# Kernel tuning notes

Hardware: AMD Instinct MI355X
Metric: run time of the kernel (lower is better)

Reference implementation:

```python
import jax, jax.numpy as jnp
import numpy as np

ATOM_DIMS = [119, 4, 12, 12, 10, 6, 6, 2, 2]
OFFSETS = jnp.asarray(np.concatenate([[0], np.cumsum(ATOM_DIMS)[:-1]]), dtype=jnp.int64)
TOTAL_ROWS = int(np.sum(ATOM_DIMS))  # 173
EPS = 1e-5
PROCESSING_STEPS = 4


def setup_inputs() -> dict:
    key = jax.random.key(0)
    ks = jax.random.split(key, 20)
    N, E, G, H, ENC = 262144, 524288, 8192, 256, 128
    x = jax.random.randint(ks[0], (N, 9), 0, 2)
    edge_index = jax.random.randint(ks[1], (2, E), 0, N)
    batch = jnp.sort(jax.random.randint(ks[2], (N,), 0, G))
    s = 0.05
    inp = {
        'x': x, 'edge_index': edge_index, 'batch': batch, 'n_graphs': G,
        'atom_emb': jax.random.normal(ks[3], (TOTAL_ROWS, H)) * s,
        'W1': jax.random.normal(ks[4], (H, H)) * s, 'b1': jnp.zeros((H,)),
        'W2': jax.random.normal(ks[5], (H, H)) * s, 'b2': jnp.zeros((H,)),
        'W3': jax.random.normal(ks[6], (H, H)) * s, 'b3': jnp.zeros((H,)),
        'gamma': jnp.ones((H,)), 'beta': jnp.zeros((H,)),
        'Wi': jax.random.normal(ks[7], (4 * H, 2 * H)) * s,
        'Wh': jax.random.normal(ks[8], (4 * H, H)) * s,
        'bi': jnp.zeros((4 * H,)), 'bh': jnp.zeros((4 * H,)),
        'lin1_W': jax.random.normal(ks[9], (ENC, 2 * H)) * s, 'lin1_b': jnp.zeros((ENC,)),
        'lin2_W': jax.random.normal(ks[10], (1, ENC)) * s, 'lin2_b': jnp.zeros((1,)),
    }
    return inp


def _gcn_conv(h, W, b, src, tgt, dinv, n_nodes):
    # GCNConv: linear, then D^-1/2 (A+I) D^-1/2 aggregation, then bias
    hw = h @ W.T
    norm = dinv[src] * dinv[tgt]                      # [E]
    agg = jax.ops.segment_sum(hw[src] * norm[:, None], tgt, num_segments=n_nodes)
    agg = agg + hw * (dinv * dinv)[:, None]           # self-loop term
    return agg + b


def _batchnorm(h, gamma, beta):
    mu = jnp.mean(h, axis=0)
    var = jnp.mean((h - mu) ** 2, axis=0)
    return (h - mu) * jax.lax.rsqrt(var + EPS) * gamma + beta


def _set2set(h, batch, n_graphs, Wi, Wh, bi, bh):
    G, H = n_graphs, h.shape[1]
    q_star = jnp.zeros((G, 2 * H), dtype=h.dtype)
    hs = jnp.zeros((G, H), dtype=h.dtype)
    cs = jnp.zeros((G, H), dtype=h.dtype)
    for _ in range(PROCESSING_STEPS):
        gates = q_star @ Wi.T + hs @ Wh.T + bi + bh   # [G, 4H], torch gate order i,f,g,o
        i, f, g, o = jnp.split(gates, 4, axis=1)
        cs = jax.nn.sigmoid(f) * cs + jax.nn.sigmoid(i) * jnp.tanh(g)
        hs = jax.nn.sigmoid(o) * jnp.tanh(cs)
        q = hs                                        # [G, H]
        e = jnp.sum(h * q[batch], axis=1)             # [N]
        m = jax.ops.segment_max(e, batch, num_segments=G)
        ee = jnp.exp(e - m[batch])
        z = jax.ops.segment_sum(ee, batch, num_segments=G)
        a = ee / z[batch]                             # scatter-softmax
        r = jax.ops.segment_sum(a[:, None] * h, batch, num_segments=G)
        q_star = jnp.concatenate([q, r], axis=1)
    return q_star


def reference(x, edge_index, batch, n_graphs, atom_emb, W1, b1, W2, b2, W3, b3,
              gamma, beta, Wi, Wh, bi, bh, lin1_W, lin1_b, lin2_W, lin2_b):
    N = x.shape[0]
    src, tgt = edge_index[0], edge_index[1]
    # AtomEncoder: sum of per-column embeddings via one offset-gather
    embed = jnp.sum(atom_emb[x + OFFSETS[None, :]], axis=1)     # [N, H]
    # gcn_norm degrees (with self loops)
    deg = jax.ops.segment_sum(jnp.ones_like(tgt, dtype=embed.dtype), tgt, num_segments=N) + 1.0
    dinv = jax.lax.rsqrt(deg)
    out = jax.nn.relu(_gcn_conv(embed, W1, b1, src, tgt, dinv, N))
    out = _batchnorm(out, gamma, beta)
    out = jax.nn.relu(_gcn_conv(out, W2, b2, src, tgt, dinv, N))
    out = _batchnorm(out, gamma, beta)
    out = _gcn_conv(out, W3, b3, src, tgt, dinv, N)
    out = _set2set(out, batch, n_graphs, Wi, Wh, bi, bh)        # [G, 2H]
    out = out @ lin1_W.T + lin1_b
    out = out @ lin2_W.T + lin2_b
    return jax.nn.sigmoid(out)
```

## Files before the change

### kernel.cpp

```cpp
#include <hip/hip_runtime.h>
#include <hip/hip_bf16.h>
#include <math.h>

using u16 = unsigned short;
typedef __attribute__((ext_vector_type(8))) short short8;
typedef __attribute__((ext_vector_type(8))) _Float16 half8;
typedef __attribute__((ext_vector_type(4))) float f32x4;
typedef __attribute__((ext_vector_type(4))) u16 u16x4;

__device__ __constant__ int c_OFF[9] = {0, 119, 123, 135, 147, 157, 163, 169, 171};

__device__ __forceinline__ float h2f(u16 u) {
    _Float16 h;
    __builtin_memcpy(&h, &u, 2);
    return (float)h;
}
__device__ __forceinline__ u16 f2h(float f) {
    _Float16 h = (_Float16)f;
    u16 u;
    __builtin_memcpy(&u, &h, 2);
    return u;
}
__device__ __forceinline__ float sigf(float x) { return 1.f / (1.f + expf(-x)); }

__global__ void k_diagf(float* out, int G, float val) {
    int i = blockIdx.x * 256 + threadIdx.x;
    if (i < G) out[i] = val;
}

__global__ void k_zero_f32(float* p, int n) {
    int i = blockIdx.x * 256 + threadIdx.x;
    if (i < n) p[i] = 0.f;
}
__global__ void k_zero_u16(u16* p, int n) {
    int i = blockIdx.x * 256 + threadIdx.x;
    if (i < n) p[i] = 0;
}
__global__ void k_zero_int(int* p, int n) {
    int i = blockIdx.x * 256 + threadIdx.x;
    if (i < n) p[i] = 0;
}

__global__ void k_cvtW(const float* __restrict__ src, u16* __restrict__ dst, int n) {
    int i = blockIdx.x * 256 + threadIdx.x;
    if (i < n) dst[i] = f2h(src[i]);
}

__global__ __launch_bounds__(256) void k_embed(const int* __restrict__ x,
                                               const float* __restrict__ emb,
                                               u16* __restrict__ out, int N) {
    __shared__ int rows[72];
    int nb = blockIdx.x * 8;
    int tid = threadIdx.x;
    if (tid < 72) rows[tid] = x[(size_t)nb * 9 + tid] + c_OFF[tid % 9];
    __syncthreads();
    int ln = tid >> 5;
    int c8 = (tid & 31) * 8;
    float s0 = 0.f, s1 = 0.f, s2 = 0.f, s3 = 0.f, s4 = 0.f, s5 = 0.f, s6 = 0.f, s7 = 0.f;
#pragma unroll
    for (int c = 0; c < 9; ++c) {
        int r = rows[ln * 9 + c];
        f32x4 a = *(const f32x4*)&emb[r * 256 + c8];
        f32x4 b = *(const f32x4*)&emb[r * 256 + c8 + 4];
        s0 += a[0]; s1 += a[1]; s2 += a[2]; s3 += a[3];
        s4 += b[0]; s5 += b[1]; s6 += b[2]; s7 += b[3];
    }
    short8 o;
    o[0] = (short)f2h(s0); o[1] = (short)f2h(s1); o[2] = (short)f2h(s2); o[3] = (short)f2h(s3);
    o[4] = (short)f2h(s4); o[5] = (short)f2h(s5); o[6] = (short)f2h(s6); o[7] = (short)f2h(s7);
    *(short8*)&out[(size_t)(nb + ln) * 256 + c8] = o;
}

__global__ void k_gstart(const int* __restrict__ batch, int* __restrict__ gstart, int N, int G) {
    int i = blockIdx.x * 256 + threadIdx.x;
    if (i >= N) return;
    int b = batch[i];
    if (i == 0) {
        for (int g = 0; g <= b; ++g) gstart[g] = 0;
    } else {
        int p = batch[i - 1];
        for (int g = p + 1; g <= b; ++g) gstart[g] = i;
    }
    if (i == N - 1) {
        for (int g = b + 1; g <= G; ++g) gstart[g] = N;
    }
}

__global__ void k_count(const int* __restrict__ tgt, int* rp, int E) {
    int e = blockIdx.x * 256 + threadIdx.x;
    if (e < E) atomicAdd(&rp[tgt[e]], 1);
}

__global__ void k_dinv(const int* __restrict__ cnt, float* __restrict__ dinv, int N) {
    int i = blockIdx.x * 256 + threadIdx.x;
    if (i < N) dinv[i] = rsqrtf((float)cnt[i] + 1.f);
}

__global__ void k_scan1(int* __restrict__ rp, int* __restrict__ bsum, int N) {
    int t = threadIdx.x;
    int base = blockIdx.x * 1024 + t * 4;
    int v0 = 0, v1 = 0, v2 = 0, v3 = 0;
    if (base + 3 < N) {
        v0 = rp[base]; v1 = rp[base + 1]; v2 = rp[base + 2]; v3 = rp[base + 3];
    } else {
        if (base < N) v0 = rp[base];
        if (base + 1 < N) v1 = rp[base + 1];
        if (base + 2 < N) v2 = rp[base + 2];
    }
    int s = v0 + v1 + v2 + v3;
    int lane = t & 63, w = t >> 6;
    int x = s;
    for (int o = 1; o < 64; o <<= 1) {
        int y = __shfl_up(x, o, 64);
        if (lane >= o) x += y;
    }
    __shared__ int wsum[4];
    if (lane == 63) wsum[w] = x;
    __syncthreads();
    int woff = 0;
    for (int i = 0; i < w; ++i) woff += wsum[i];
    int excl = woff + x - s;
    if (base < N) rp[base] = excl;
    if (base + 1 < N) rp[base + 1] = excl + v0;
    if (base + 2 < N) rp[base + 2] = excl + v0 + v1;
    if (base + 3 < N) rp[base + 3] = excl + v0 + v1 + v2;
    if (t == 255) bsum[blockIdx.x] = wsum[0] + wsum[1] + wsum[2] + wsum[3];
}

__global__ void k_scan2(int* bsum, int nb) {
    int t = threadIdx.x;
    int s = (t < nb) ? bsum[t] : 0;
    int lane = t & 63, w = t >> 6;
    int x = s;
    for (int o = 1; o < 64; o <<= 1) {
        int y = __shfl_up(x, o, 64);
        if (lane >= o) x += y;
    }
    __shared__ int wsum[4];
    if (lane == 63) wsum[w] = x;
    __syncthreads();
    int woff = 0;
    for (int i = 0; i < w; ++i) woff += wsum[i];
    if (t < nb) bsum[t] = woff + x - s;
}

__global__ void k_scan3(int* __restrict__ rp, const int* __restrict__ bsum, int N) {
    int i = blockIdx.x * 256 + threadIdx.x;
    if (i < N) rp[i] += bsum[i >> 10];
}

__global__ void k_fill(const int* __restrict__ src, const int* __restrict__ tgt,
                       int* __restrict__ rp, const float* __restrict__ dinv,
                       int2* __restrict__ est, int E) {
    int e = blockIdx.x * 256 + threadIdx.x;
    if (e < E) {
        int t = tgt[e];
        int s = src[e];
        int p = atomicAdd(&rp[t], 1);
        est[p] = make_int2(s, __float_as_int(dinv[s] * dinv[t]));
    }
}

__global__ __launch_bounds__(256, 3) void k_gemm(const u16* __restrict__ p0, int rs0,
                                                 const u16* __restrict__ p1, int rs1,
                                                 const u16* __restrict__ W,
                                                 const float* __restrict__ cvec,
                                                 u16* __restrict__ out, int N) {
    __shared__ u16 As[64][260];
    __shared__ u16 Ws[256][36];
    int r0 = blockIdx.x * 64;
    int tid = threadIdx.x, lane = tid & 63, w = tid >> 6;
#pragma unroll
    for (int i = 0; i < 8; ++i) {
        int chunk = i * 256 + tid;
        int r = chunk >> 5, c8 = chunk & 31;
        const u16* sp = (c8 < 16) ? &p0[(size_t)(r0 + r) * rs0 + c8 * 8]
                                  : &p1[(size_t)(r0 + r) * rs1 + (c8 - 16) * 8];
        *(short8*)&As[r][c8 * 8] = *(const short8*)sp;
    }
    f32x4 acc[16];
#pragma unroll
    for (int o = 0; o < 16; ++o) acc[o] = f32x4{0.f, 0.f, 0.f, 0.f};
    for (int k0 = 0; k0 < 256; k0 += 32) {
        __syncthreads();
#pragma unroll
        for (int i = 0; i < 4; ++i) {
            int chunk = i * 256 + tid;
            int r = chunk >> 2, c8 = chunk & 3;
            *(short8*)&Ws[r][c8 * 8] = *(const short8*)&W[(size_t)r * 256 + k0 + c8 * 8];
        }
        __syncthreads();
        half8 af = *(const half8*)&As[w * 16 + (lane & 15)][k0 + (lane >> 4) * 8];
#pragma unroll
        for (int o = 0; o < 16; ++o) {
            half8 wf = *(const half8*)&Ws[o * 16 + (lane & 15)][(lane >> 4) * 8];
            acc[o] = __builtin_amdgcn_mfma_f32_16x16x32_f16(af, wf, acc[o], 0, 0, 0);
        }
    }
    __syncthreads();
#pragma unroll
    for (int o = 0; o < 16; ++o) {
        int col = o * 16 + (lane & 15);
        float cv = cvec ? cvec[col] : 0.f;
#pragma unroll
        for (int r = 0; r < 4; ++r) {
            int row = w * 16 + (lane >> 4) * 4 + r;
            As[row][col] = f2h(acc[o][r] + cv);
        }
    }
    __syncthreads();
#pragma unroll
    for (int i = 0; i < 8; ++i) {
        int chunk = i * 256 + tid;
        int r = chunk >> 5, c8 = chunk & 31;
        *(short8*)&out[(size_t)(r0 + r) * 256 + c8 * 8] = *(const short8*)&As[r][c8 * 8];
    }
}

template <bool RS>
__global__ __launch_bounds__(256) void k_aggh(const u16* __restrict__ src, int srs,
                                              u16* __restrict__ dst, int drs,
                                              const int* __restrict__ rp,
                                              const int2* __restrict__ est,
                                              const float* __restrict__ dinv,
                                              const float* __restrict__ biasH,
                                              float* __restrict__ statS,
                                              float* __restrict__ statQ, int N) {
    int l = threadIdx.x & 15;
    int sub = blockIdx.x * 16 + (threadIdx.x >> 4);
    int nsub = gridDim.x * 16;
    float bv[8];
#pragma unroll
    for (int k = 0; k < 8; ++k) bv[k] = biasH[l * 8 + k];
    float ss[8] = {}, qq[8] = {};
    for (int n = sub; n < N; n += nsub) {
        int start = n ? rp[n - 1] : 0;
        int end = rp[n];
        float dn = dinv[n];
        short8 hv = *(const short8*)&src[(size_t)n * srs + l * 8];
        float a[8];
#pragma unroll
        for (int k = 0; k < 8; ++k) a[k] = h2f((u16)hv[k]) * dn * dn + bv[k];
        int j = start;
        for (; j + 1 < end; j += 2) {
            int2 e0 = est[j], e1 = est[j + 1];
            float n0 = __int_as_float(e0.y), n1 = __int_as_float(e1.y);
            short8 v0 = *(const short8*)&src[(size_t)e0.x * srs + l * 8];
            short8 v1 = *(const short8*)&src[(size_t)e1.x * srs + l * 8];
#pragma unroll
            for (int k = 0; k < 8; ++k) a[k] += h2f((u16)v0[k]) * n0 + h2f((u16)v1[k]) * n1;
        }
        if (j < end) {
            int2 e0 = est[j];
            float n0 = __int_as_float(e0.y);
            short8 v0 = *(const short8*)&src[(size_t)e0.x * srs + l * 8];
#pragma unroll
            for (int k = 0; k < 8; ++k) a[k] += h2f((u16)v0[k]) * n0;
        }
        short8 o;
#pragma unroll
        for (int k = 0; k < 8; ++k) {
            if (RS) {
                a[k] = fmaxf(a[k], 0.f);
                ss[k] += a[k];
                qq[k] += a[k] * a[k];
            }
            o[k] = (short)f2h(a[k]);
        }
        *(short8*)&dst[(size_t)n * drs + l * 8] = o;
    }
    if (RS) {
        __shared__ float sh[256];
        int t = threadIdx.x;
        sh[t] = 0.f;
        __syncthreads();
#pragma unroll
        for (int k = 0; k < 8; ++k) {
            atomicAdd(&sh[l * 8 + k], ss[k]);
            atomicAdd(&sh[128 + l * 8 + k], qq[k]);
        }
        __syncthreads();
        if (t < 128)
            atomicAdd(&statS[t], sh[t]);
        else
            atomicAdd(&statQ[t - 128], sh[t]);
    }
}

__global__ void k_copyh(const u16* __restrict__ src, u16* __restrict__ dst, int N) {
    int i = blockIdx.x * 256 + threadIdx.x;
    if (i >= N * 16) return;
    int n = i >> 4, c8 = (i & 15) * 8;
    *(short8*)&dst[(size_t)n * 128 + c8] = *(const short8*)&src[(size_t)n * 256 + c8];
}

__global__ void k_bnparam(const float* __restrict__ stats, const float* __restrict__ gamma,
                          const float* __restrict__ beta, float* __restrict__ st, int N) {
    int d = threadIdx.x;
    float inv = 1.f / (float)N;
    float mu = stats[d] * inv;
    float var = fmaxf(stats[256 + d] * inv - mu * mu, 0.f);
    float sc = gamma[d] * rsqrtf(var + 1e-5f);
    st[d] = sc;
    st[256 + d] = beta[d] - mu * sc;
}

__global__ void k_fold(const float* __restrict__ W, const float* __restrict__ st,
                       u16* __restrict__ Wp, float* __restrict__ cvec) {
    __shared__ float red[256];
    int o = blockIdx.x, k = threadIdx.x;
    float w = W[o * 256 + k];
    Wp[o * 256 + k] = f2h(w * st[k]);
    red[k] = w * st[256 + k];
    __syncthreads();
    for (int s = 128; s > 0; s >>= 1) {
        if (k < s) red[k] += red[k + s];
        __syncthreads();
    }
    if (k == 0) cvec[o] = red[0];
}

__global__ __launch_bounds__(256, 2) void k_gemmf(const u16* __restrict__ A,
                                                  const u16* __restrict__ W,
                                                  const float* __restrict__ cvec,
                                                  u16* __restrict__ C, int M, int K, int O) {
    const int PAD = 8;
    __shared__ u16 As[128][64 + PAD];
    __shared__ u16 Ws[128][64 + PAD];
    int tM = blockIdx.x, tO = blockIdx.y;
    int tid = threadIdx.x;
    int lane = tid & 63, wid = tid >> 6;
    int wM = wid & 1, wO = wid >> 1;
    f32x4 acc[4][4] = {};
    size_t rowA0 = (size_t)tM * 128, rowW0 = (size_t)tO * 128;
    for (int k0 = 0; k0 < K; k0 += 64) {
#pragma unroll
        for (int i = 0; i < 4; ++i) {
            int chunk = tid + i * 256;
            int r = chunk >> 3, c16 = chunk & 7;
            *(short8*)&As[r][c16 * 8] = *(const short8*)&A[(rowA0 + r) * K + k0 + c16 * 8];
            *(short8*)&Ws[r][c16 * 8] = *(const short8*)&W[(rowW0 + r) * K + k0 + c16 * 8];
        }
        __syncthreads();
#pragma unroll
        for (int ks = 0; ks < 2; ++ks) {
            half8 af[4], wf[4];
#pragma unroll
            for (int m = 0; m < 4; ++m)
                af[m] = *(const half8*)&As[wM * 64 + m * 16 + (lane & 15)][ks * 32 + (lane >> 4) * 8];
#pragma unroll
            for (int o = 0; o < 4; ++o)
                wf[o] = *(const half8*)&Ws[wO * 64 + o * 16 + (lane & 15)][ks * 32 + (lane >> 4) * 8];
#pragma unroll
            for (int m = 0; m < 4; ++m)
#pragma unroll
                for (int o = 0; o < 4; ++o)
                    acc[m][o] = __builtin_amdgcn_mfma_f32_16x16x32_f16(af[m], wf[o], acc[m][o], 0, 0, 0);
        }
        __syncthreads();
    }
#pragma unroll
    for (int m = 0; m < 4; ++m) {
        int R0 = tM * 128 + wM * 64 + m * 16 + (lane >> 4) * 4;
#pragma unroll
        for (int o = 0; o < 4; ++o) {
            int Cc = tO * 128 + wO * 64 + o * 16 + (lane & 15);
            float cv = cvec[Cc];
#pragma unroll
            for (int r = 0; r < 4; ++r)
                C[(size_t)(R0 + r) * O + Cc] = f2h(acc[m][o][r] + cv);
        }
    }
}

__global__ void k_wcat(const float* __restrict__ Wi, const float* __restrict__ Wh,
                       const float* __restrict__ bi, const float* __restrict__ bh,
                       u16* __restrict__ Wcat, float* __restrict__ bcat) {
    int o = blockIdx.x;
    int t = threadIdx.x;
    for (int c = t; c < 512; c += 256) Wcat[(size_t)o * 768 + c] = f2h(Wi[(size_t)o * 512 + c]);
    if (t < 256) Wcat[(size_t)o * 768 + 512 + t] = f2h(Wh[(size_t)o * 256 + t]);
    if (t == 0) bcat[o] = bi[o] + bh[o];
}

__global__ void k_lstm(const u16* __restrict__ gates, float* __restrict__ cs,
                       float* __restrict__ hsb, u16* __restrict__ qsh, int G) {
    int idx = blockIdx.x * 256 + threadIdx.x;
    if (idx >= G * 256) return;
    int g = idx >> 8, d = idx & 255;
    const u16* gt = &gates[(size_t)g * 1024];
    float gi = h2f(gt[d]), gf = h2f(gt[256 + d]), gg = h2f(gt[512 + d]), go = h2f(gt[768 + d]);
    float c = sigf(gf) * cs[idx] + sigf(gi) * tanhf(gg);
    float hh = sigf(go) * tanhf(c);
    cs[idx] = c;
    hsb[idx] = hh;
    u16 hb = f2h(hh);
    qsh[(size_t)g * 768 + d] = hb;
    qsh[(size_t)g * 768 + 512 + d] = hb;
}

__global__ __launch_bounds__(256) void k_attn2(const u16* __restrict__ h3,
                                               const float* __restrict__ hs,
                                               const int* __restrict__ gstart,
                                               u16* __restrict__ qsh, int G) {
    int wid = threadIdx.x >> 6, lane = threadIdx.x & 63;
    int g = blockIdx.x * 4 + wid;
    if (g >= G) return;
    int start = gstart[g], end = gstart[g + 1];

    f32x4 q = *(const f32x4*)&hs[(size_t)g * 256 + lane * 4];
    float m = -INFINITY, z = 0.f;
    float r0a = 0.f, r1a = 0.f, r2a = 0.f, r3a = 0.f;

    for (int c0 = start; c0 < end; c0 += 256) {
        int cn = min(256, end - c0);
        float e0 = 0.f, e1 = 0.f, e2 = 0.f, e3 = 0.f;
        float mc = m;

        auto pass1 = [&](int rr, float& ev) {
            int b = c0 + rr * 64;
            int nr = min(64, end - b);
            for (int ii = 0; ii < nr; ++ii) {
                u16x4 hv = *(const u16x4*)&h3[(size_t)(b + ii) * 256 + lane * 4];
                float e = h2f(hv[0]) * q[0] + h2f(hv[1]) * q[1] + h2f(hv[2]) * q[2] + h2f(hv[3]) * q[3];
                e += __shfl_xor(e, 32, 64);
                e += __shfl_xor(e, 16, 64);
                e += __shfl_xor(e, 8, 64);
                e += __shfl_xor(e, 4, 64);
                e += __shfl_xor(e, 2, 64);
                e += __shfl_xor(e, 1, 64);
                if (lane == ii) ev = e;
                mc = fmaxf(mc, e);
            }
        };
        pass1(0, e0);
        pass1(1, e1);
        pass1(2, e2);
        pass1(3, e3);

        float rf = (m == -INFINITY) ? 0.f : expf(m - mc);
        float zc = 0.f;
        e0 = (lane < cn) ? expf(e0 - mc) : 0.f;
        zc += e0;
        e1 = (64 + lane < cn) ? expf(e1 - mc) : 0.f;
        zc += e1;
        e2 = (128 + lane < cn) ? expf(e2 - mc) : 0.f;
        zc += e2;
        e3 = (192 + lane < cn) ? expf(e3 - mc) : 0.f;
        zc += e3;
        zc += __shfl_xor(zc, 32, 64);
        zc += __shfl_xor(zc, 16, 64);
        zc += __shfl_xor(zc, 8, 64);
        zc += __shfl_xor(zc, 4, 64);
        zc += __shfl_xor(zc, 2, 64);
        zc += __shfl_xor(zc, 1, 64);
        z = z * rf + zc;
        r0a *= rf; r1a *= rf; r2a *= rf; r3a *= rf;

        auto pass2 = [&](int rr, float ev) {
            int b = c0 + rr * 64;
            int nr = min(64, end - b);
            for (int ii = 0; ii < nr; ++ii) {
                float w = __shfl(ev, ii, 64);
                u16x4 hv = *(const u16x4*)&h3[(size_t)(b + ii) * 256 + lane * 4];
                r0a += w * h2f(hv[0]);
                r1a += w * h2f(hv[1]);
                r2a += w * h2f(hv[2]);
                r3a += w * h2f(hv[3]);
            }
        };
        pass2(0, e0);
        pass2(1, e1);
        pass2(2, e2);
        pass2(3, e3);
        m = mc;
    }
    float inv = (end > start) ? 1.f / fmaxf(z, 1e-30f) : 0.f;
    u16x4 o;
    o[0] = f2h(r0a * inv);
    o[1] = f2h(r1a * inv);
    o[2] = f2h(r2a * inv);
    o[3] = f2h(r3a * inv);
    *(u16x4*)&qsh[(size_t)g * 768 + 256 + lane * 4] = o;
}

__global__ void k_wfold(const float* __restrict__ l1W, const float* __restrict__ l1b,
                        const float* __restrict__ l2W, const float* __restrict__ l2b,
                        float* __restrict__ weff) {
    int c = blockIdx.x * 256 + threadIdx.x;
    if (c < 512) {
        float s = 0.f;
        for (int t = 0; t < 128; ++t) s += l2W[t] * l1W[(size_t)t * 512 + c];
        weff[c] = s;
    }
    if (c == 0) {
        float b = l2b[0];
        for (int t = 0; t < 128; ++t) b += l2W[t] * l1b[t];
        weff[512] = b;
    }
}

__global__ __launch_bounds__(256) void k_final2(const u16* __restrict__ qsh,
                                                const float* __restrict__ weff,
                                                float* __restrict__ out, int G) {
    __shared__ float wsm[513];
    int tid = threadIdx.x;
    for (int j = tid; j < 513; j += 256) wsm[j] = weff[j];
    __syncthreads();
    int g = blockIdx.x * 4 + (tid >> 6);
    int lane = tid & 63;
    if (g >= G) return;
    const u16* qp = &qsh[(size_t)g * 768];
    float s = 0.f;
#pragma unroll
    for (int j = 0; j < 8; ++j) s += h2f(qp[lane * 8 + j]) * wsm[lane * 8 + j];
    for (int off = 32; off; off >>= 1) s += __shfl_xor(s, off, 64);
    if (lane == 0) out[g] = sigf(s + wsm[512]);
}

extern "C" void kernel_launch(void* const* d_in, const int* in_sizes, int n_in,
                              void* d_out, int out_size, void* d_ws, size_t ws_size,
                              hipStream_t stream) {
    const int* x = (const int*)d_in[0];
    const int* ei = (const int*)d_in[1];
    const int* batch = (const int*)d_in[2];
    const float* atom_emb = (const float*)d_in[4];
    const float* W1 = (const float*)d_in[5];
    const float* b1 = (const float*)d_in[6];
    const float* W2 = (const float*)d_in[7];
    const float* b2 = (const float*)d_in[8];
    const float* W3 = (const float*)d_in[9];
    const float* b3 = (const float*)d_in[10];
    const float* gamma = (const float*)d_in[11];
    const float* beta = (const float*)d_in[12];
    const float* Wi = (const float*)d_in[13];
    const float* Wh = (const float*)d_in[14];
    const float* bi = (const float*)d_in[15];
    const float* bh = (const float*)d_in[16];
    const float* l1W = (const float*)d_in[17];
    const float* l1b = (const float*)d_in[18];
    const float* l2W = (const float*)d_in[19];
    const float* l2b = (const float*)d_in[20];

    const int N = in_sizes[0] / 9;
    const int E = in_sizes[1] / 2;
    const int G = out_size;
    const int* srcp = ei;
    const int* tgtp = ei + E;

    char* ws = (char*)d_ws;
    size_t off = 0;
    auto alloc = [&](size_t bytes) -> void* {
        void* p = ws + off;
        off += (bytes + 255) & ~(size_t)255;
        return p;
    };
    u16* X = (u16*)alloc((size_t)N * 256 * 2);
    int* rp = (int*)alloc((size_t)N * 4);
    int2* est = (int2*)alloc((size_t)E * 8);
    float* dinv = (float*)alloc((size_t)N * 4);
    int* gstart = (int*)alloc((size_t)(G + 1) * 4);
    float* stats = (float*)alloc(512 * 4);
    float* stbuf = (float*)alloc(512 * 4);
    float* cvec = (float*)alloc(256 * 4);
    u16* Wp = (u16*)alloc(256 * 256 * 2);
    int* bsum = (int*)alloc(1024 * 4);
    float* weff = (float*)alloc(513 * 4);
    size_t offR = off;

    size_t o2 = offR;
    auto alloc2 = [&](size_t bytes) -> void* {
        void* p = ws + o2;
        o2 += (bytes + 255) & ~(size_t)255;
        return p;
    };
    u16* Wcat = (u16*)alloc2((size_t)1024 * 768 * 2);
    float* bcat = (float*)alloc2(1024 * 4);
    u16* qsh = (u16*)alloc2((size_t)G * 768 * 2);
    u16* gates = (u16*)alloc2((size_t)G * 1024 * 2);
    float* hsb = (float*)alloc2((size_t)G * 256 * 4);
    float* csb = (float*)alloc2((size_t)G * 256 * 4);
    size_t s2sR = o2 - offR;

    size_t halfB = ((size_t)N * 128 * 2 + 255) & ~(size_t)255;
    size_t need = offR + (halfB > s2sR ? halfB : s2sR);
    if (ws_size < need) {
        k_diagf<<<(G + 255) / 256, 256, 0, stream>>>((float*)d_out, G, 12345.0f);
        return;
    }
    u16* Y = (u16*)(ws + offR);

    k_embed<<<N / 8, 256, 0, stream>>>(x, atom_emb, X, N);
    k_gstart<<<(N + 255) / 256, 256, 0, stream>>>(batch, gstart, N, G);
    k_zero_int<<<(N + 255) / 256, 256, 0, stream>>>(rp, N);
    k_count<<<(E + 255) / 256, 256, 0, stream>>>(tgtp, rp, E);
    k_dinv<<<(N + 255) / 256, 256, 0, stream>>>(rp, dinv, N);
    int nb1 = (N + 1023) / 1024;
    k_scan1<<<nb1, 256, 0, stream>>>(rp, bsum, N);
    k_scan2<<<1, 256, 0, stream>>>(bsum, nb1);
    k_scan3<<<(N + 255) / 256, 256, 0, stream>>>(rp, bsum, N);
    k_fill<<<(E + 255) / 256, 256, 0, stream>>>(srcp, tgtp, rp, dinv, est, E);

    int gipb = N / 64;
    int cpb = (N * 16 + 255) / 256;
    const int AGGB = 4096;

    k_cvtW<<<256, 256, 0, stream>>>(W1, Wp, 65536);
    k_zero_f32<<<2, 256, 0, stream>>>(stats, 512);
    k_gemm<<<gipb, 256, 0, stream>>>(X, 256, X + 128, 256, Wp, nullptr, X, N);
    k_aggh<true><<<AGGB, 256, 0, stream>>>(X, 256, Y, 128, rp, est, dinv, b1, stats, stats + 256, N);
    k_aggh<true><<<AGGB, 256, 0, stream>>>(X + 128, 256, X, 256, rp, est, dinv, b1 + 128, stats + 128, stats + 384, N);
    k_bnparam<<<1, 256, 0, stream>>>(stats, gamma, beta, stbuf, N);

    k_fold<<<256, 256, 0, stream>>>(W2, stbuf, Wp, cvec);
    k_zero_f32<<<2, 256, 0, stream>>>(stats, 512);
    k_gemm<<<gipb, 256, 0, stream>>>(Y, 128, X, 256, Wp, cvec, X, N);
    k_aggh<true><<<AGGB, 256, 0, stream>>>(X, 256, Y, 128, rp, est, dinv, b2, stats, stats + 256, N);
    k_aggh<true><<<AGGB, 256, 0, stream>>>(X + 128, 256, X, 256, rp, est, dinv, b2 + 128, stats + 128, stats + 384, N);
    k_bnparam<<<1, 256, 0, stream>>>(stats, gamma, beta, stbuf, N);

    k_fold<<<256, 256, 0, stream>>>(W3, stbuf, Wp, cvec);
    k_gemm<<<gipb, 256, 0, stream>>>(Y, 128, X, 256, Wp, cvec, X, N);
    k_copyh<<<cpb, 256, 0, stream>>>(X, Y, N);
    k_aggh<false><<<AGGB, 256, 0, stream>>>(Y, 128, X, 256, rp, est, dinv, b3, nullptr, nullptr, N);
    k_copyh<<<cpb, 256, 0, stream>>>(X + 128, Y, N);
    k_aggh<false><<<AGGB, 256, 0, stream>>>(Y, 128, X + 128, 256, rp, est, dinv, b3 + 128, nullptr, nullptr, N);

    k_wcat<<<1024, 256, 0, stream>>>(Wi, Wh, bi, bh, Wcat, bcat);
    k_zero_u16<<<(G * 768 + 255) / 256, 256, 0, stream>>>(qsh, G * 768);
    k_zero_f32<<<(G * 256 + 255) / 256, 256, 0, stream>>>(csb, G * 256);
    dim3 ggates(G / 128, 8);
    for (int s = 0; s < 4; ++s) {
        k_gemmf<<<ggates, 256, 0, stream>>>(qsh, Wcat, bcat, gates, G, 768, 1024);
        k_lstm<<<(G * 256 + 255) / 256, 256, 0, stream>>>(gates, csb, hsb, qsh, G);
        k_attn2<<<(G + 3) / 4, 256, 0, stream>>>(X, hsb, gstart, qsh, G);
    }
    k_wfold<<<2, 256, 0, stream>>>(l1W, l1b, l2W, l2b, weff);
    k_final2<<<(G + 3) / 4, 256, 0, stream>>>(qsh, weff, (float*)d_out, G);
}
```

Baseline: 1.507 ms.

## Assign four consecutive nodes per aggregation group and drop layer-3 copy kernels

The aggregation kernel now gives each 16-lane group four consecutive nodes instead of a grid-stride loop. This reuses the row-pointer boundary between nodes and sizes the grid to N/64 blocks. When the workspace is large enough, the separate Y buffer stays live alongside the set2set buffers, so the layer-3 aggregation writes its low half into Y and skips the two k_copyh passes. k_attn2 then reads the two halves from separate base pointers and strides. This removes two full N×128 copies, at the cost of a larger workspace requirement and extra per-lane address selection in attention.

New measurement: 1.469 ms. 2.5% less time.

```diff
diff --git a/kernel.cpp b/kernel.cpp
--- a/kernel.cpp
+++ b/kernel.cpp
@@ -228,35 +228,39 @@
                                               float* __restrict__ statQ, int N) {
     int l = threadIdx.x & 15;
     int sub = blockIdx.x * 16 + (threadIdx.x >> 4);
-    int nsub = gridDim.x * 16;
+    int n0 = sub * 4;
+    if (n0 >= N) return;
     float bv[8];
 #pragma unroll
     for (int k = 0; k < 8; ++k) bv[k] = biasH[l * 8 + k];
     float ss[8] = {}, qq[8] = {};
-    for (int n = sub; n < N; n += nsub) {
-        int start = n ? rp[n - 1] : 0;
-        int end = rp[n];
+    int rA = n0 ? rp[n0 - 1] : 0;
+#pragma unroll
+    for (int t = 0; t < 4; ++t) {
+        int n = n0 + t;
+        int rB = rp[n];
         float dn = dinv[n];
         short8 hv = *(const short8*)&src[(size_t)n * srs + l * 8];
         float a[8];
 #pragma unroll
         for (int k = 0; k < 8; ++k) a[k] = h2f((u16)hv[k]) * dn * dn + bv[k];
-        int j = start;
-        for (; j + 1 < end; j += 2) {
+        int j = rA;
+        for (; j + 1 < rB; j += 2) {
             int2 e0 = est[j], e1 = est[j + 1];
-            float n0 = __int_as_float(e0.y), n1 = __int_as_float(e1.y);
+            float n0f = __int_as_float(e0.y), n1f = __int_as_float(e1.y);
             short8 v0 = *(const short8*)&src[(size_t)e0.x * srs + l * 8];
             short8 v1 = *(const short8*)&src[(size_t)e1.x * srs + l * 8];
 #pragma unroll
-            for (int k = 0; k < 8; ++k) a[k] += h2f((u16)v0[k]) * n0 + h2f((u16)v1[k]) * n1;
-        }
-        if (j < end) {
+            for (int k = 0; k < 8; ++k) a[k] += h2f((u16)v0[k]) * n0f + h2f((u16)v1[k]) * n1f;
+        }
+        if (j < rB) {
             int2 e0 = est[j];
-            float n0 = __int_as_float(e0.y);
+            float n0f = __int_as_float(e0.y);
             short8 v0 = *(const short8*)&src[(size_t)e0.x * srs + l * 8];
 #pragma unroll
-            for (int k = 0; k < 8; ++k) a[k] += h2f((u16)v0[k]) * n0;
-        }
+            for (int k = 0; k < 8; ++k) a[k] += h2f((u16)v0[k]) * n0f;
+        }
+        rA = rB;
         short8 o;
 #pragma unroll
         for (int k = 0; k < 8; ++k) {
@@ -399,7 +403,8 @@
     qsh[(size_t)g * 768 + 512 + d] = hb;
 }
 
-__global__ __launch_bounds__(256) void k_attn2(const u16* __restrict__ h3,
+__global__ __launch_bounds__(256) void k_attn2(const u16* __restrict__ lo, int lstr,
+                                               const u16* __restrict__ hi, int hstr,
                                                const float* __restrict__ hs,
                                                const int* __restrict__ gstart,
                                                u16* __restrict__ qsh, int G) {
@@ -408,6 +413,10 @@
     if (g >= G) return;
     int start = gstart[g], end = gstart[g + 1];
 
+    const u16* base = (lane < 32) ? lo : hi;
+    size_t stride = (lane < 32) ? lstr : hstr;
+    int coff = (lane < 32) ? lane * 4 : (lane - 32) * 4;
+
     f32x4 q = *(const f32x4*)&hs[(size_t)g * 256 + lane * 4];
     float m = -INFINITY, z = 0.f;
     float r0a = 0.f, r1a = 0.f, r2a = 0.f, r3a = 0.f;
@@ -421,7 +430,7 @@
             int b = c0 + rr * 64;
             int nr = min(64, end - b);
             for (int ii = 0; ii < nr; ++ii) {
-                u16x4 hv = *(const u16x4*)&h3[(size_t)(b + ii) * 256 + lane * 4];
+                u16x4 hv = *(const u16x4*)&base[(size_t)(b + ii) * stride + coff];
                 float e = h2f(hv[0]) * q[0] + h2f(hv[1]) * q[1] + h2f(hv[2]) * q[2] + h2f(hv[3]) * q[3];
                 e += __shfl_xor(e, 32, 64);
                 e += __shfl_xor(e, 16, 64);
@@ -462,7 +471,7 @@
             int nr = min(64, end - b);
             for (int ii = 0; ii < nr; ++ii) {
                 float w = __shfl(ev, ii, 64);
-                u16x4 hv = *(const u16x4*)&h3[(size_t)(b + ii) * 256 + lane * 4];
+                u16x4 hv = *(const u16x4*)&base[(size_t)(b + ii) * stride + coff];
                 r0a += w * h2f(hv[0]);
                 r1a += w * h2f(hv[1]);
                 r2a += w * h2f(hv[2]);
@@ -481,7 +490,8 @@
     o[1] = f2h(r1a * inv);
     o[2] = f2h(r2a * inv);
     o[3] = f2h(r3a * inv);
-    *(u16x4*)&qsh[(size_t)g * 768 + 256 + lane * 4] = o;
+    int qcol = (lane < 32) ? lane * 4 : 128 + (lane - 32) * 4;
+    *(u16x4*)&qsh[(size_t)g * 768 + 256 + qcol] = o;
 }
 
 __global__ void k_wfold(const float* __restrict__ l1W, const float* __restrict__ l1b,
@@ -568,7 +578,29 @@
     float* weff = (float*)alloc(513 * 4);
     size_t offR = off;
 
-    size_t o2 = offR;
+    size_t halfB = ((size_t)N * 128 * 2 + 255) & ~(size_t)255;
+    size_t s2sR = 0;
+    {
+        size_t t = 0;
+        auto sz = [&](size_t b) { t += (b + 255) & ~(size_t)255; };
+        sz((size_t)1024 * 768 * 2);
+        sz(1024 * 4);
+        sz((size_t)G * 768 * 2);
+        sz((size_t)G * 1024 * 2);
+        sz((size_t)G * 256 * 4);
+        sz((size_t)G * 256 * 4);
+        s2sR = t;
+    }
+    size_t needA = offR + halfB + s2sR;
+    size_t needB = offR + (halfB > s2sR ? halfB : s2sR);
+    bool tierA = ws_size >= needA;
+    if (!tierA && ws_size < needB) {
+        k_diagf<<<(G + 255) / 256, 256, 0, stream>>>((float*)d_out, G, 12345.0f);
+        return;
+    }
+    u16* Y = (u16*)(ws + offR);
+    size_t s2sBase = tierA ? offR + halfB : offR;
+    size_t o2 = s2sBase;
     auto alloc2 = [&](size_t bytes) -> void* {
         void* p = ws + o2;
         o2 += (bytes + 255) & ~(size_t)255;
@@ -580,15 +612,6 @@
     u16* gates = (u16*)alloc2((size_t)G * 1024 * 2);
     float* hsb = (float*)alloc2((size_t)G * 256 * 4);
     float* csb = (float*)alloc2((size_t)G * 256 * 4);
-    size_t s2sR = o2 - offR;
-
-    size_t halfB = ((size_t)N * 128 * 2 + 255) & ~(size_t)255;
-    size_t need = offR + (halfB > s2sR ? halfB : s2sR);
-    if (ws_size < need) {
-        k_diagf<<<(G + 255) / 256, 256, 0, stream>>>((float*)d_out, G, 12345.0f);
-        return;
-    }
-    u16* Y = (u16*)(ws + offR);
 
     k_embed<<<N / 8, 256, 0, stream>>>(x, atom_emb, X, N);
     k_gstart<<<(N + 255) / 256, 256, 0, stream>>>(batch, gstart, N, G);
@@ -603,28 +626,37 @@
 
     int gipb = N / 64;
     int cpb = (N * 16 + 255) / 256;
-    const int AGGB = 4096;
+    int aggb = (N / 4 + 15) / 16;
 
     k_cvtW<<<256, 256, 0, stream>>>(W1, Wp, 65536);
     k_zero_f32<<<2, 256, 0, stream>>>(stats, 512);
     k_gemm<<<gipb, 256, 0, stream>>>(X, 256, X + 128, 256, Wp, nullptr, X, N);
-    k_aggh<true><<<AGGB, 256, 0, stream>>>(X, 256, Y, 128, rp, est, dinv, b1, stats, stats + 256, N);
-    k_aggh<true><<<AGGB, 256, 0, stream>>>(X + 128, 256, X, 256, rp, est, dinv, b1 + 128, stats + 128, stats + 384, N);
+    k_aggh<true><<<aggb, 256, 0, stream>>>(X, 256, Y, 128, rp, est, dinv, b1, stats, stats + 256, N);
+    k_aggh<true><<<aggb, 256, 0, stream>>>(X + 128, 256, X, 256, rp, est, dinv, b1 + 128, stats + 128, stats + 384, N);
     k_bnparam<<<1, 256, 0, stream>>>(stats, gamma, beta, stbuf, N);
 
     k_fold<<<256, 256, 0, stream>>>(W2, stbuf, Wp, cvec);
     k_zero_f32<<<2, 256, 0, stream>>>(stats, 512);
     k_gemm<<<gipb, 256, 0, stream>>>(Y, 128, X, 256, Wp, cvec, X, N);
-    k_aggh<true><<<AGGB, 256, 0, stream>>>(X, 256, Y, 128, rp, est, dinv, b2, stats, stats + 256, N);
-    k_aggh<true><<<AGGB, 256, 0, stream>>>(X + 128, 256, X, 256, rp, est, dinv, b2 + 128, stats + 128, stats + 384, N);
+    k_aggh<true><<<aggb, 256, 0, stream>>>(X, 256, Y, 128, rp, est, dinv, b2, stats, stats + 256, N);
+    k_aggh<true><<<aggb, 256, 0, stream>>>(X + 128, 256, X, 256, rp, est, dinv, b2 + 128, stats + 128, stats + 384, N);
     k_bnparam<<<1, 256, 0, stream>>>(stats, gamma, beta, stbuf, N);
 
     k_fold<<<256, 256, 0, stream>>>(W3, stbuf, Wp, cvec);
     k_gemm<<<gipb, 256, 0, stream>>>(Y, 128, X, 256, Wp, cvec, X, N);
-    k_copyh<<<cpb, 256, 0, stream>>>(X, Y, N);
-    k_aggh<false><<<AGGB, 256, 0, stream>>>(Y, 128, X, 256, rp, est, dinv, b3, nullptr, nullptr, N);
-    k_copyh<<<cpb, 256, 0, stream>>>(X + 128, Y, N);
-    k_aggh<false><<<AGGB, 256, 0, stream>>>(Y, 128, X + 128, 256, rp, est, dinv, b3 + 128, nullptr, nullptr, N);
+    const u16 *h3lo, *h3hi;
+    int h3ls, h3hs;
+    if (tierA) {
+        k_aggh<false><<<aggb, 256, 0, stream>>>(X, 256, Y, 128, rp, est, dinv, b3, nullptr, nullptr, N);
+        k_aggh<false><<<aggb, 256, 0, stream>>>(X + 128, 256, X, 256, rp, est, dinv, b3 + 128, nullptr, nullptr, N);
+        h3lo = Y; h3ls = 128; h3hi = X; h3hs = 256;
+    } else {
+        k_copyh<<<cpb, 256, 0, stream>>>(X, Y, N);
+        k_aggh<false><<<aggb, 256, 0, stream>>>(Y, 128, X, 256, rp, est, dinv, b3, nullptr, nullptr, N);
+        k_copyh<<<cpb, 256, 0, stream>>>(X + 128, Y, N);
+        k_aggh<false><<<aggb, 256, 0, stream>>>(Y, 128, X + 128, 256, rp, est, dinv, b3 + 128, nullptr, nullptr, N);
+        h3lo = X; h3ls = 256; h3hi = X + 128; h3hs = 256;
+    }
 
     k_wcat<<<1024, 256, 0, stream>>>(Wi, Wh, bi, bh, Wcat, bcat);
     k_zero_u16<<<(G * 768 + 255) / 256, 256, 0, stream>>>(qsh, G * 768);
@@ -633,7 +665,7 @@
     for (int s = 0; s < 4; ++s) {
         k_gemmf<<<ggates, 256, 0, stream>>>(qsh, Wcat, bcat, gates, G, 768, 1024);
         k_lstm<<<(G * 256 + 255) / 256, 256, 0, stream>>>(gates, csb, hsb, qsh, G);
-        k_attn2<<<(G + 3) / 4, 256, 0, stream>>>(X, hsb, gstart, qsh, G);
+        k_attn2<<<(G + 3) / 4, 256, 0, stream>>>(h3lo, h3ls, h3hi, h3hs, hsb, gstart, qsh, G);
     }
     k_wfold<<<2, 256, 0, stream>>>(l1W, l1b, l2W, l2b, weff);
     k_final2<<<(G + 3) / 4, 256, 0, stream>>>(qsh, weff, (float*)d_out, G);
```
